# Kernel optimization log

Measured on AMD Instinct MI355X. Metric: run time of the kernel, lower is better.

Reference implementation:

```python
import jax, jax.numpy as jnp
import numpy as np

B, N, HD = 4, 16384, 1024
H, M = 8, 32
D = HD // H  # 128


def setup_inputs() -> dict:
    key = jax.random.key(0)
    ks = jax.random.split(key, 8)
    std = 0.02
    x = jax.random.normal(ks[0], (B, N, HD), dtype=jnp.float32)
    wt_kv_weight = jax.random.normal(ks[1], (2 * HD, HD), dtype=jnp.float32) * std
    wt_kv_bias = jnp.zeros((2 * HD,), dtype=jnp.float32)
    wtq = jax.random.normal(ks[2], (H, M, D), dtype=jnp.float32) * std
    wtq_bias = jnp.zeros((H, M), dtype=jnp.float32)  # registered buffer, zeros
    qkv_proj = jax.random.normal(ks[3], (H, D, 3 * D), dtype=jnp.float32) * std
    out_weight = jax.random.normal(ks[4], (HD, HD), dtype=jnp.float32) * std
    out_bias = jnp.zeros((HD,), dtype=jnp.float32)
    return {
        'x': x,
        'wt_kv_weight': wt_kv_weight,
        'wt_kv_bias': wt_kv_bias,
        'wtq': wtq,
        'wtq_bias': wtq_bias,
        'qkv_proj': qkv_proj,
        'out_weight': out_weight,
        'out_bias': out_bias,
    }


def reference(x, wt_kv_weight, wt_kv_bias, wtq, wtq_bias, qkv_proj, out_weight, out_bias):
    b, n, hd = x.shape
    h, m, d = wtq.shape
    # wt_kv_proj: Linear(hd, 2hd); torch Linear: x @ W.T + b
    kv = x @ wt_kv_weight.T + wt_kv_bias  # [b, n, 2hd]
    xk, xv = jnp.split(kv, 2, axis=-1)
    xk = xk.reshape(b, n, h, d).transpose(0, 2, 1, 3)  # b h n d
    xv = xv.reshape(b, n, h, d).transpose(0, 2, 1, 3)  # b h n d
    # qk_norm=False -> no normalize
    slice_scores = jnp.einsum('hmd,bhnd->bhmn', wtq, xk)
    slice_weights = jax.nn.softmax(slice_scores, axis=-2)  # softmax over slice axis m
    bias = wtq_bias[..., None]  # [h, m, 1]
    slice_token = jnp.einsum('bhmn,bhnd->bhmd', slice_weights, xv)
    slice_norm = jnp.sum(slice_weights, axis=-1, keepdims=True)  # [b,h,m,1]
    slice_token = slice_token / (slice_norm + 1e-5)
    qkv_token = jnp.einsum('bhmd,hde->bhme', slice_token, qkv_proj)  # e = 3d
    q_tok, k_tok, v_tok = jnp.split(qkv_token, 3, axis=-1)
    scale = d ** (-0.5)
    dots = jnp.einsum('bhqd,bhkd->bhqk', q_tok, k_tok) * scale
    attn_weights = jax.nn.softmax(dots, axis=-1)
    out_token = jnp.einsum('bhqk,bhkd->bhqd', attn_weights, v_tok)
    # scatter back via slice weights
    out = jnp.einsum('bhmd,bhmn->bhnd', out_token, slice_weights)
    out = out.transpose(0, 2, 1, 3).reshape(b, n, hd)
    out = out @ out_weight.T + out_bias  # to_out linear (dropout=0)
    temperature = jnp.asarray(1.0, dtype=x.dtype)
    return (out, slice_weights, temperature, bias, attn_weights)
```

## Files before the change

### kernel.cpp

```cpp
#include <hip/hip_runtime.h>
#include <hip/hip_bf16.h>
#include <stdint.h>

#define BB 4
#define NN 16384
#define HDIM 1024
#define HH 8
#define MM 32
#define DD 128

typedef unsigned int u32;
typedef unsigned short u16;
typedef __attribute__((ext_vector_type(8))) short short8;
typedef __attribute__((ext_vector_type(4))) float f32x4;

__device__ __forceinline__ float bf2f(u16 v) {
    union { u32 u; float f; } c; c.u = ((u32)v) << 16; return c.f;
}
__device__ __forceinline__ u16 f2bf(float f) {
    union { float f; u32 u; } c; c.f = f;
    u32 r = c.u + 0x7fffu + ((c.u >> 16) & 1u);
    return (u16)(r >> 16);
}

__device__ __forceinline__ void gload16(const u16* g, u16* l) {
    __builtin_amdgcn_global_load_lds(
        (const __attribute__((address_space(1))) void*)g,
        (__attribute__((address_space(3))) void*)l, 16, 0, 0);
}

#define MFMA16(a, b, c) __builtin_amdgcn_mfma_f32_16x16x32_bf16(a, b, c, 0, 0, 0)

__global__ __launch_bounds__(256) void convert_kernel(const float* __restrict__ x,
                                                      u16* __restrict__ xb, u16* __restrict__ xbT,
                                                      const float* __restrict__ wtq_bias,
                                                      float* __restrict__ out_misc) {
    __shared__ u32 tl[128 * 65];
    const int t = threadIdx.x;
    const int eb = blockIdx.x & 7;
    const int nb = blockIdx.x >> 3;
    const size_t n0 = (size_t)nb * 128;
    const int e0 = eb * 128;

#pragma unroll 4
    for (int i = 0; i < 32; i++) {
        const int idx = t + i * 256;
        const int nl = idx >> 6, e2 = idx & 63;
        const float2 v = *(const float2*)&x[(n0 + nl) * 1024 + e0 + e2 * 2];
        const u32 pk = (u32)f2bf(v.x) | ((u32)f2bf(v.y) << 16);
        ((u32*)xb)[((n0 + nl) * 1024 + e0) / 2 + e2] = pk;
        tl[nl * 65 + e2] = pk;
    }
    __syncthreads();
    const int b = (int)(n0 >> 14);
    const int nloc = (int)(n0 & 16383);
#pragma unroll 4
    for (int i = 0; i < 32; i++) {
        const int idx = t + i * 256;
        const int el = idx >> 6, n2 = idx & 63;
        const u32 w0 = tl[(2 * n2) * 65 + (el >> 1)];
        const u32 w1 = tl[(2 * n2 + 1) * 65 + (el >> 1)];
        const int sh = (el & 1) * 16;
        const u32 o = ((w0 >> sh) & 0xffffu) | (((w1 >> sh) & 0xffffu) << 16);
        ((u32*)xbT)[((size_t)(b * 1024 + e0 + el) * 16384 + nloc + 2 * n2) >> 1] = o;
    }
    if (blockIdx.x == 0) {
        if (t == 0) out_misc[0] = 1.0f;
        if (t < HH * MM) out_misc[1 + t] = wtq_bias[t];
    }
}

__global__ __launch_bounds__(256) void wq_kernel(const float* __restrict__ wtq,
                                                 const float* __restrict__ wkv,
                                                 const float* __restrict__ bkv,
                                                 u16* __restrict__ WQb, float* __restrict__ wqbias,
                                                 u16* __restrict__ wvb) {
    __shared__ float wtql[MM * DD];
    const int ec = blockIdx.x, h = blockIdx.y, t = threadIdx.x;
    for (int i = t; i < MM * DD; i += 256) wtql[i] = wtq[(size_t)h * MM * DD + i];
    __syncthreads();
    const int m = t >> 3;
    const int e = ec * 128 + (t & 7) * 16;
    float acc[16];
#pragma unroll
    for (int j = 0; j < 16; j++) acc[j] = 0.f;
    for (int d = 0; d < DD; d++) {
        const float wv = wtql[m * DD + d];
        const float4* row = (const float4*)(wkv + (size_t)(h * DD + d) * HDIM + e);
#pragma unroll
        for (int j4 = 0; j4 < 4; j4++) {
            float4 v = row[j4];
            acc[j4 * 4 + 0] += wv * v.x; acc[j4 * 4 + 1] += wv * v.y;
            acc[j4 * 4 + 2] += wv * v.z; acc[j4 * 4 + 3] += wv * v.w;
        }
    }
    u32 pk[8];
#pragma unroll
    for (int p = 0; p < 8; p++)
        pk[p] = (u32)f2bf(acc[2 * p]) | ((u32)f2bf(acc[2 * p + 1]) << 16);
    u16* dst = WQb + (size_t)(h * MM + m) * HDIM + e;
#pragma unroll
    for (int p = 0; p < 2; p++) {
        uint4 q4; q4.x = pk[4 * p]; q4.y = pk[4 * p + 1]; q4.z = pk[4 * p + 2]; q4.w = pk[4 * p + 3];
        *(uint4*)&dst[p * 8] = q4;
    }
    if (ec == 0 && t < MM) {
        float s = 0.f;
        for (int d = 0; d < DD; d++) s += wtql[t * DD + d] * bkv[h * DD + d];
        wqbias[h * MM + t] = s;
    }
    {
        const int blk = blockIdx.y * 8 + blockIdx.x;
        const float4* src = (const float4*)(wkv + (size_t)1024 * 1024);
        for (int i = t; i < 4096; i += 256) {
            const int idx4 = blk * 4096 + i;
            float4 v = src[idx4];
            ushort4 o; o.x = f2bf(v.x); o.y = f2bf(v.y); o.z = f2bf(v.z); o.w = f2bf(v.w);
            ((ushort4*)wvb)[idx4] = o;
        }
    }
}

__global__ __launch_bounds__(512, 1) void gemm_score_sm(
        const u16* __restrict__ A, const u16* __restrict__ Bm,
        const float* __restrict__ bias,
        float* __restrict__ sw_out, u16* __restrict__ wN, u16* __restrict__ wT,
        float* __restrict__ pnorm) {
    __shared__ u16 smem[65536];
    const int t = threadIdx.x, l = t & 63, w = t >> 6;
    const int wr = w >> 2, wc = w & 3;

    const int nwg = gridDim.x, cpx = nwg >> 3, bid = blockIdx.x;
    const int tm = (bid & 7) * cpx + (bid >> 3);

    f32x4 acc[8][4];
    const f32x4 zero = {0.f, 0.f, 0.f, 0.f};
#pragma unroll
    for (int mi = 0; mi < 8; mi++)
#pragma unroll
        for (int ni = 0; ni < 4; ni++) acc[mi][ni] = zero;

    const int srow = w * 8 + (l >> 3);
    const int skel = ((l & 7) ^ ((l >> 3) & 7)) * 8;
    const u16* gA = A  + (size_t)(tm * 256 + srow) * 1024 + skel;
    const u16* gB = Bm + (size_t)srow * 1024 + skel;
    const int ldo = w * 512 + l * 8;

#define LAp(SL, H) (&smem[(SL) * 16384 + (H) * 8192])
#define LBp(SL, H) (&smem[32768 + (SL) * 16384 + (H) * 8192])
#define STAGE_A(T, H) { const u16* g_ = gA + (size_t)((H) * 128) * 1024 + (T) * 64; \
    u16* d_ = LAp((T) & 1, H) + ldo; gload16(g_, d_); gload16(g_ + (size_t)64 * 1024, d_ + 4096); }
#define STAGE_B(T, H) { const u16* g_ = gB + (size_t)((H) * 128) * 1024 + (T) * 64; \
    u16* d_ = LBp((T) & 1, H) + ldo; gload16(g_, d_); gload16(g_ + (size_t)64 * 1024, d_ + 4096); }

    const int m16 = l & 15;
    const int ck0 = (((l >> 4) + 0) ^ (l & 7)) << 3;
    const int ck1 = (((l >> 4) + 4) ^ (l & 7)) << 3;
    const int brb = (wc & 1) * 64;
    const int nT = 16;

    STAGE_A(0, 0); STAGE_A(0, 1); STAGE_B(0, 0); STAGE_B(0, 1);
    STAGE_B(1, 0); STAGE_B(1, 1);
    asm volatile("s_waitcnt vmcnt(4)" ::: "memory");
    __builtin_amdgcn_s_barrier();

    for (int kt = 0; kt < nT; ++kt) {
        const int sl = kt & 1;
        const u16* lA = LAp(sl, wr);
        const u16* lB = LBp(sl, wc >> 1);
        short8 aF[4][2], bF[4][2];

#pragma unroll
        for (int fr = 0; fr < 4; fr++) {
            aF[fr][0] = *(const short8*)&lA[(fr * 16 + m16) * 64 + ck0];
            aF[fr][1] = *(const short8*)&lA[(fr * 16 + m16) * 64 + ck1];
        }
#pragma unroll
        for (int fc = 0; fc < 2; fc++) {
            bF[fc][0] = *(const short8*)&lB[(brb + fc * 16 + m16) * 64 + ck0];
            bF[fc][1] = *(const short8*)&lB[(brb + fc * 16 + m16) * 64 + ck1];
        }
        if (kt + 1 < nT) STAGE_A(kt + 1, 0);
        __builtin_amdgcn_s_barrier();
        asm volatile("s_waitcnt lgkmcnt(0)" ::: "memory");
        __builtin_amdgcn_s_setprio(1);
#pragma unroll
        for (int kk = 0; kk < 2; kk++)
#pragma unroll
            for (int mi = 0; mi < 4; mi++) {
                acc[mi][0] = MFMA16(aF[mi][kk], bF[0][kk], acc[mi][0]);
                acc[mi][1] = MFMA16(aF[mi][kk], bF[1][kk], acc[mi][1]);
            }
        __builtin_amdgcn_s_setprio(0);
        __builtin_amdgcn_s_barrier();

#pragma unroll
        for (int fc = 2; fc < 4; fc++) {
            bF[fc][0] = *(const short8*)&lB[(brb + fc * 16 + m16) * 64 + ck0];
            bF[fc][1] = *(const short8*)&lB[(brb + fc * 16 + m16) * 64 + ck1];
        }
        if (kt + 1 < nT) STAGE_A(kt + 1, 1);
        __builtin_amdgcn_s_barrier();
        asm volatile("s_waitcnt lgkmcnt(0)" ::: "memory");
        __builtin_amdgcn_s_setprio(1);
#pragma unroll
        for (int kk = 0; kk < 2; kk++)
#pragma unroll
            for (int mi = 0; mi < 4; mi++) {
                acc[mi][2] = MFMA16(aF[mi][kk], bF[2][kk], acc[mi][2]);
                acc[mi][3] = MFMA16(aF[mi][kk], bF[3][kk], acc[mi][3]);
            }
        __builtin_amdgcn_s_setprio(0);
        __builtin_amdgcn_s_barrier();

#pragma unroll
        for (int fr = 0; fr < 4; fr++) {
            aF[fr][0] = *(const short8*)&lA[((fr + 4) * 16 + m16) * 64 + ck0];
            aF[fr][1] = *(const short8*)&lA[((fr + 4) * 16 + m16) * 64 + ck1];
        }
        if (kt + 2 < nT) STAGE_B(kt + 2, 0);
        __builtin_amdgcn_s_barrier();
        asm volatile("s_waitcnt lgkmcnt(0)" ::: "memory");
        __builtin_amdgcn_s_setprio(1);
#pragma unroll
        for (int kk = 0; kk < 2; kk++)
#pragma unroll
            for (int mi = 0; mi < 4; mi++) {
                acc[4 + mi][0] = MFMA16(aF[mi][kk], bF[0][kk], acc[4 + mi][0]);
                acc[4 + mi][1] = MFMA16(aF[mi][kk], bF[1][kk], acc[4 + mi][1]);
            }
        __builtin_amdgcn_s_setprio(0);
        __builtin_amdgcn_s_barrier();

        if (kt + 2 < nT) STAGE_B(kt + 2, 1);
        __builtin_amdgcn_s_barrier();
        __builtin_amdgcn_s_setprio(1);
#pragma unroll
        for (int kk = 0; kk < 2; kk++)
#pragma unroll
            for (int mi = 0; mi < 4; mi++) {
                acc[4 + mi][2] = MFMA16(aF[mi][kk], bF[2][kk], acc[4 + mi][2]);
                acc[4 + mi][3] = MFMA16(aF[mi][kk], bF[3][kk], acc[4 + mi][3]);
            }
        __builtin_amdgcn_s_setprio(0);
        if (kt < nT - 1) {
            if (kt + 2 < nT) asm volatile("s_waitcnt vmcnt(4)" ::: "memory");
            else             asm volatile("s_waitcnt vmcnt(0)" ::: "memory");
            __builtin_amdgcn_s_barrier();
        }
    }
#undef STAGE_A
#undef STAGE_B
#undef LAp
#undef LBp

    __syncthreads();
    const int cr = (l >> 4) * 4;
    const int cc = l & 15;
#pragma unroll
    for (int ni = 0; ni < 4; ni++) {
        const int hm = wc * 64 + ni * 16 + cc;
        const float bv = bias[hm];
#pragma unroll
        for (int mi = 0; mi < 8; mi++) {
            const int nb_ = wr * 128 + mi * 16 + cr;
            u32 lo = (u32)f2bf(acc[mi][ni][0] + bv) | ((u32)f2bf(acc[mi][ni][1] + bv) << 16);
            u32 hi = (u32)f2bf(acc[mi][ni][2] + bv) | ((u32)f2bf(acc[mi][ni][3] + bv) << 16);
            uint2 pk; pk.x = lo; pk.y = hi;
            *(uint2*)&smem[hm * 256 + (((nb_ >> 2) ^ (hm & 63)) << 2)] = pk;
        }
    }
    __syncthreads();

    const int b = tm >> 6, g = tm & 63;
    const int n_ = t & 255, hs = (t >> 8) * 4;
    const size_t gn = (size_t)g * 256 + n_;
    for (int h = hs; h < hs + 4; h++) {
        float sv[MM];
#pragma unroll
        for (int m = 0; m < MM; m++) {
            const int hm = h * 32 + m;
            sv[m] = bf2f(smem[hm * 256 + (((n_ >> 2) ^ (hm & 63)) << 2) + (n_ & 3)]);
        }
        float mx = sv[0];
#pragma unroll
        for (int m = 1; m < MM; m++) mx = fmaxf(mx, sv[m]);
        float sum = 0.f;
#pragma unroll
        for (int m = 0; m < MM; m++) { sv[m] = __expf(sv[m] - mx); sum += sv[m]; }
        const float inv = 1.f / sum;
        u32 wpk[16];
#pragma unroll
        for (int m = 0; m < MM; m++) {
            const float wv = sv[m] * inv;
            const int hm = h * 32 + m;
            const size_t row = (size_t)(b * 256 + hm);
            sw_out[row * NN + gn] = wv;
            const u16 wb = f2bf(wv);
            wN[row * NN + gn] = wb;
            smem[hm * 256 + (((n_ >> 2) ^ (hm & 63)) << 2) + (n_ & 3)] = wb;
            if (m & 1) wpk[m >> 1] |= ((u32)wb << 16); else wpk[m >> 1] = (u32)wb;
        }
        u16* wrow = wT + ((size_t)(b * NN) + gn) * 256 + h * 32;
#pragma unroll
        for (int p = 0; p < 4; p++) {
            uint4 q4; q4.x = wpk[4 * p]; q4.y = wpk[4 * p + 1]; q4.z = wpk[4 * p + 2]; q4.w = wpk[4 * p + 3];
            *(uint4*)&wrow[p * 8] = q4;
        }
    }
    __syncthreads();

    {
        const int hm2 = t >> 1, half = t & 1;
        float s = 0.f;
        for (int j = 0; j < 128; j++) {
            const int n2 = half * 128 + j;
            s += bf2f(smem[hm2 * 256 + (((n2 >> 2) ^ (hm2 & 63)) << 2) + (n2 & 3)]);
        }
        s += __shfl_xor(s, 1);
        if (half == 0)
            pnorm[((size_t)(b * 8 + (hm2 >> 5)) * 64 + g) * MM + (hm2 & 31)] = s;
    }
}

template<int MODE>
__global__ __launch_bounds__(512, 1) void gemm_nt(
        const u16* __restrict__ A, const u16* __restrict__ Bm,
        const float* __restrict__ bias, void* __restrict__ Cout,
        int NCols, int Kd, int ldk, int ntn, int bofs, int bshift,
        long long bstrideB, long long kCstride) {
    __shared__ u16 ldsA[2][2][8192];
    __shared__ u16 ldsB[2][2][8192];
    const int t = threadIdx.x, l = t & 63, w = t >> 6;
    const int wr = w >> 2, wc = w & 3;

    const int nwg = gridDim.x, cpx = nwg >> 3, bid = blockIdx.x;
    const int swz = (nwg >= 8) ? ((bid & 7) * cpx + (bid >> 3)) : bid;
    const int tm = swz / ntn, tn = swz % ntn;
    const int ks = blockIdx.y;
    const u16* Bb = Bm + (size_t)(tm >> bshift) * bstrideB;

    f32x4 acc[8][4];
    const f32x4 zero = {0.f, 0.f, 0.f, 0.f};
#pragma unroll
    for (int mi = 0; mi < 8; mi++)
#pragma unroll
        for (int ni = 0; ni < 4; ni++) acc[mi][ni] = zero;

    const int srow = w * 8 + (l >> 3);
    const int skel = ((l & 7) ^ ((l >> 3) & 7)) * 8;
    const u16* gA = A  + (size_t)(tm * 256 + srow) * ldk + (size_t)ks * Kd + skel;
    const u16* gB = Bb + (size_t)(tn * 256 + srow) * ldk + (size_t)ks * Kd + skel;
    const int ldo = w * 512 + l * 8;

#define STAGE_A(T, H) { const u16* g_ = gA + (size_t)((H) * 128) * ldk + (T) * 64; \
    u16* d_ = &ldsA[(T) & 1][H][ldo]; gload16(g_, d_); gload16(g_ + (size_t)64 * ldk, d_ + 4096); }
#define STAGE_B(T, H) { const u16* g_ = gB + (size_t)((H) * 128) * ldk + (T) * 64; \
    u16* d_ = &ldsB[(T) & 1][H][ldo]; gload16(g_, d_); gload16(g_ + (size_t)64 * ldk, d_ + 4096); }

    const int m16 = l & 15;
    const int ck0 = (((l >> 4) + 0) ^ (l & 7)) << 3;
    const int ck1 = (((l >> 4) + 4) ^ (l & 7)) << 3;
    const int brb = (wc & 1) * 64;
    const int nT = Kd >> 6;

    STAGE_A(0, 0); STAGE_A(0, 1); STAGE_B(0, 0); STAGE_B(0, 1);
    STAGE_B(1, 0); STAGE_B(1, 1);
    asm volatile("s_waitcnt vmcnt(4)" ::: "memory");
    __builtin_amdgcn_s_barrier();

    for (int kt = 0; kt < nT; ++kt) {
        const int sl = kt & 1;
        const u16* lA = ldsA[sl][wr];
        const u16* lB = ldsB[sl][wc >> 1];
        short8 aF[4][2], bF[4][2];

#pragma unroll
        for (int fr = 0; fr < 4; fr++) {
            aF[fr][0] = *(const short8*)&lA[(fr * 16 + m16) * 64 + ck0];
            aF[fr][1] = *(const short8*)&lA[(fr * 16 + m16) * 64 + ck1];
        }
#pragma unroll
        for (int fc = 0; fc < 2; fc++) {
            bF[fc][0] = *(const short8*)&lB[(brb + fc * 16 + m16) * 64 + ck0];
            bF[fc][1] = *(const short8*)&lB[(brb + fc * 16 + m16) * 64 + ck1];
        }
        if (kt + 1 < nT) STAGE_A(kt + 1, 0);
        __builtin_amdgcn_s_barrier();
        asm volatile("s_waitcnt lgkmcnt(0)" ::: "memory");
        __builtin_amdgcn_s_setprio(1);
#pragma unroll
        for (int kk = 0; kk < 2; kk++)
#pragma unroll
            for (int mi = 0; mi < 4; mi++) {
                acc[mi][0] = MFMA16(aF[mi][kk], bF[0][kk], acc[mi][0]);
                acc[mi][1] = MFMA16(aF[mi][kk], bF[1][kk], acc[mi][1]);
            }
        __builtin_amdgcn_s_setprio(0);
        __builtin_amdgcn_s_barrier();

#pragma unroll
        for (int fc = 2; fc < 4; fc++) {
            bF[fc][0] = *(const short8*)&lB[(brb + fc * 16 + m16) * 64 + ck0];
            bF[fc][1] = *(const short8*)&lB[(brb + fc * 16 + m16) * 64 + ck1];
        }
        if (kt + 1 < nT) STAGE_A(kt + 1, 1);
        __builtin_amdgcn_s_barrier();
        asm volatile("s_waitcnt lgkmcnt(0)" ::: "memory");
        __builtin_amdgcn_s_setprio(1);
#pragma unroll
        for (int kk = 0; kk < 2; kk++)
#pragma unroll
            for (int mi = 0; mi < 4; mi++) {
                acc[mi][2] = MFMA16(aF[mi][kk], bF[2][kk], acc[mi][2]);
                acc[mi][3] = MFMA16(aF[mi][kk], bF[3][kk], acc[mi][3]);
            }
        __builtin_amdgcn_s_setprio(0);
        __builtin_amdgcn_s_barrier();

#pragma unroll
        for (int fr = 0; fr < 4; fr++) {
            aF[fr][0] = *(const short8*)&lA[((fr + 4) * 16 + m16) * 64 + ck0];
            aF[fr][1] = *(const short8*)&lA[((fr + 4) * 16 + m16) * 64 + ck1];
        }
        if (kt + 2 < nT) STAGE_B(kt + 2, 0);
        __builtin_amdgcn_s_barrier();
        asm volatile("s_waitcnt lgkmcnt(0)" ::: "memory");
        __builtin_amdgcn_s_setprio(1);
#pragma unroll
        for (int kk = 0; kk < 2; kk++)
#pragma unroll
            for (int mi = 0; mi < 4; mi++) {
                acc[4 + mi][0] = MFMA16(aF[mi][kk], bF[0][kk], acc[4 + mi][0]);
                acc[4 + mi][1] = MFMA16(aF[mi][kk], bF[1][kk], acc[4 + mi][1]);
            }
        __builtin_amdgcn_s_setprio(0);
        __builtin_amdgcn_s_barrier();

        if (kt + 2 < nT) STAGE_B(kt + 2, 1);
        __builtin_amdgcn_s_barrier();
        __builtin_amdgcn_s_setprio(1);
#pragma unroll
        for (int kk = 0; kk < 2; kk++)
#pragma unroll
            for (int mi = 0; mi < 4; mi++) {
                acc[4 + mi][2] = MFMA16(aF[mi][kk], bF[2][kk], acc[4 + mi][2]);
                acc[4 + mi][3] = MFMA16(aF[mi][kk], bF[3][kk], acc[4 + mi][3]);
            }
        __builtin_amdgcn_s_setprio(0);
        if (kt < nT - 1) {
            if (kt + 2 < nT) asm volatile("s_waitcnt vmcnt(4)" ::: "memory");
            else             asm volatile("s_waitcnt vmcnt(0)" ::: "memory");
            __builtin_amdgcn_s_barrier();
        }
    }
#undef STAGE_A
#undef STAGE_B

    const int cr = (l >> 4) * 4;
    const int cc = l & 15;
    if (MODE == 2) {
        u16* Cp = (u16*)Cout + (size_t)ks * kCstride;
#pragma unroll
        for (int ni = 0; ni < 4; ni++) {
            const int col = tn * 256 + wc * 64 + ni * 16 + cc;
            const float bv = bias ? bias[col] : 0.0f;
#pragma unroll
            for (int mi = 0; mi < 8; mi++) {
                const int row0 = tm * 256 + wr * 128 + mi * 16 + cr;
#pragma unroll
                for (int q = 0; q < 4; q++)
                    Cp[(size_t)(row0 + q) * NCols + col] = f2bf(acc[mi][ni][q] + bv);
            }
        }
    } else {
        float* Cp = (float*)Cout + (size_t)ks * kCstride;
#pragma unroll
        for (int ni = 0; ni < 4; ni++) {
            const int col = tn * 256 + wc * 64 + ni * 16 + cc;
            const float bv = bias ? bias[col] : 0.0f;
#pragma unroll
            for (int mi = 0; mi < 8; mi++) {
                const int row0 = tm * 256 + wr * 128 + mi * 16 + cr;
#pragma unroll
                for (int q = 0; q < 4; q++)
                    Cp[(size_t)(row0 + q) * NCols + col] = acc[mi][ni][q] + bv;
            }
        }
    }
}

__global__ __launch_bounds__(256, 2) void gemm_small(
        const u16* __restrict__ A, const u16* __restrict__ Bm,
        const float* __restrict__ bias, float* __restrict__ Cout,
        int Ncols, int Kds, int ldk, int ntn, int bshift,
        long long bstrideB, long long kCstride) {
    __shared__ u16 lds_a[128 * 32];
    __shared__ u16 lds_b[128 * 32];
    const int t = threadIdx.x, l = t & 63, w = t >> 6;
    const int wr = w >> 1, wc = w & 1;

    const int nwg = gridDim.x, cpx = nwg >> 3, bid = blockIdx.x;
    const int swz = (nwg >= 8) ? ((bid & 7) * cpx + (bid >> 3)) : bid;
    const int tm = swz / ntn, tn = swz % ntn;
    const int ks = blockIdx.y;
    const u16* Bb = Bm + (size_t)(tm >> bshift) * bstrideB;

    f32x4 acc[4][4];
    const f32x4 zero = {0.f, 0.f, 0.f, 0.f};
#pragma unroll
    for (int mi = 0; mi < 4; mi++)
#pragma unroll
        for (int ni = 0; ni < 4; ni++) acc[mi][ni] = zero;

    const int srow = w * 32 + (l >> 2);
    const int scol = (l & 3) * 8;
    const u16* ga = A  + (size_t)(tm * 128 + srow) * ldk + (size_t)ks * Kds + scol;
    const u16* gb = Bb + (size_t)(tn * 128 + srow) * ldk + (size_t)ks * Kds + scol;
    u16* la = &lds_a[(w * 32) * 32];
    u16* lb = &lds_b[(w * 32) * 32];
    const size_t rstep = (size_t)16 * ldk;

    const int nK = Kds >> 5;
    const int kg = (l >> 4) * 8;
    const int ra = wr * 64 + (l & 15);
    const int rb = wc * 64 + (l & 15);

    for (int kt = 0; kt < nK; kt++) {
        __syncthreads();
        const int ko = kt << 5;
        gload16(ga + ko,         la);
        gload16(ga + ko + rstep, la + 16 * 32);
        gload16(gb + ko,         lb);
        gload16(gb + ko + rstep, lb + 16 * 32);
        __syncthreads();

        short8 af[4], bfr[4];
#pragma unroll
        for (int mi = 0; mi < 4; mi++) af[mi] = *(const short8*)&lds_a[(ra + mi * 16) * 32 + kg];
#pragma unroll
        for (int ni = 0; ni < 4; ni++) bfr[ni] = *(const short8*)&lds_b[(rb + ni * 16) * 32 + kg];
#pragma unroll
        for (int mi = 0; mi < 4; mi++)
#pragma unroll
            for (int ni = 0; ni < 4; ni++)
                acc[mi][ni] = MFMA16(af[mi], bfr[ni], acc[mi][ni]);
    }

    float* Cp = Cout + (size_t)ks * kCstride;
#pragma unroll
    for (int ni = 0; ni < 4; ni++) {
        const int col = tn * 128 + wc * 64 + ni * 16 + (l & 15);
        const float bv = bias ? bias[col] : 0.0f;
#pragma unroll
        for (int mi = 0; mi < 4; mi++) {
            const int row0 = tm * 128 + wr * 64 + mi * 16 + ((l >> 4) << 2);
#pragma unroll
            for (int q = 0; q < 4; q++)
                Cp[(size_t)(row0 + q) * Ncols + col] = acc[mi][ni][q] + bv;
        }
    }
}

__global__ __launch_bounds__(256) void sum_U(const u16* __restrict__ U_part, u16* __restrict__ U2) {
    const int i = blockIdx.x * 256 + threadIdx.x;
    float4 s = make_float4(0.f, 0.f, 0.f, 0.f);
    for (int ks = 0; ks < 16; ks++) {
        const ushort4 v = ((const ushort4*)(U_part + (size_t)ks * 1048576))[i];
        s.x += bf2f(v.x); s.y += bf2f(v.y); s.z += bf2f(v.z); s.w += bf2f(v.w);
    }
    const int r = i >> 8, e4 = i & 255;
    const int b = r >> 8, h = (r >> 5) & 7, m = r & 31;
    const int r2 = h * 128 + b * 32 + m;
    ushort4 o; o.x = f2bf(s.x); o.y = f2bf(s.y); o.z = f2bf(s.z); o.w = f2bf(s.w);
    ((ushort4*)U2)[r2 * 256 + e4] = o;
}

__global__ __launch_bounds__(256) void st_fix(const float* __restrict__ C2,
                                              const float* __restrict__ pnorm,
                                              const float* __restrict__ bkv,
                                              u16* __restrict__ st_red) {
    __shared__ float norm[MM];
    const int bh = blockIdx.x, b = bh >> 3, h = bh & 7, t = threadIdx.x;
    if (t < MM) {
        float s = 0.f;
        for (int g = 0; g < 64; g++) s += pnorm[((size_t)bh * 64 + g) * MM + t];
        norm[t] = s;
    }
    __syncthreads();
#pragma unroll
    for (int i = 0; i < 16; i++) {
        const int idx = t * 16 + i;
        const int m = idx >> 7, d = idx & 127;
        const float nv = norm[m];
        float c = 0.f;
        const size_t off = (size_t)(h * 128 + d) * 128 + b * 32 + m;
#pragma unroll
        for (int ks = 0; ks < 8; ks++) c += C2[(size_t)ks * 131072 + off];
        const float v = (c + bkv[1024 + h * 128 + d] * nv) / (nv + 1e-5f);
        st_red[(size_t)bh * 4096 + idx] = f2bf(v);
    }
}

__global__ __launch_bounds__(256) void qt_kernel(const u16* __restrict__ st_red,
                                                 const float* __restrict__ qkvp,
                                                 float* __restrict__ qt_g) {
    __shared__ u16 st_lds[MM * DD];
    const int es = blockIdx.x, bh = blockIdx.y, h = bh & 7, t = threadIdx.x;
    {
        const uint4* src = (const uint4*)(st_red + (size_t)bh * 4096);
        ((uint4*)st_lds)[t] = src[t];
        ((uint4*)st_lds)[t + 256] = src[t + 256];
    }
    __syncthreads();
    const float* qw = qkvp + (size_t)h * DD * 384;
#pragma unroll
    for (int i = 0; i < 4; i++) {
        const int idx = t + i * 256;
        const int m = idx >> 5, el = idx & 31;
        const int e = es * 32 + el;
        float s = 0.f;
        for (int d = 0; d < DD; d++) s += bf2f(st_lds[m * DD + d]) * qw[d * 384 + e];
        qt_g[((size_t)bh * MM + m) * 384 + e] = s;
    }
}

__global__ void finalize2_kernel(const float* __restrict__ qt_g,
                                 float* __restrict__ attn_out, float* __restrict__ otw) {
    __shared__ float qt[MM * 384];
    __shared__ float dots[MM * MM];
    const int bh = blockIdx.x, t = threadIdx.x;

#pragma unroll
    for (int i = 0; i < 48; i++) qt[t + i * 256] = qt_g[(size_t)bh * 12288 + t + i * 256];
    __syncthreads();
    const float scale = 0.08838834764831845f;
#pragma unroll
    for (int i = 0; i < 4; i++) {
        int idx = t * 4 + i;
        int qi = idx >> 5, kj = idx & 31;
        float s = 0.f;
        for (int d = 0; d < DD; d++) s += qt[qi * 384 + d] * qt[kj * 384 + 128 + d];
        dots[idx] = s * scale;
    }
    __syncthreads();
    if (t < MM) {
        float mx = -1e30f;
        float ex[MM];
#pragma unroll
        for (int j = 0; j < MM; j++) mx = fmaxf(mx, dots[t * MM + j]);
        float sm = 0.f;
#pragma unroll
        for (int j = 0; j < MM; j++) { ex[j] = __expf(dots[t * MM + j] - mx); sm += ex[j]; }
        float inv = 1.f / sm;
#pragma unroll
        for (int j = 0; j < MM; j++) {
            float v = ex[j] * inv;
            dots[t * MM + j] = v;
            attn_out[((size_t)bh * MM + t) * MM + j] = v;
        }
    }
    __syncthreads();
#pragma unroll
    for (int i = 0; i < 16; i++) {
        int e = t + i * 256;
        int m = e >> 7, d = e & 127;
        float s = 0.f;
#pragma unroll
        for (int j = 0; j < MM; j++) s += dots[m * MM + j] * qt[j * 384 + 256 + d];
        otw[(size_t)bh * 4096 + e] = s;
    }
}

__global__ __launch_bounds__(256) void zmat_kernel(const float* __restrict__ otw,
                                                   const float* __restrict__ outw,
                                                   u16* __restrict__ Zt) {
    __shared__ float ot_lds[MM * DD];
    const int bh = blockIdx.y, b = bh >> 3, h = bh & 7;
    const int es = blockIdx.x;
    const int t = threadIdx.x;
    for (int i = t; i < MM * DD; i += 256) ot_lds[i] = otw[(size_t)bh * 4096 + i];
    __syncthreads();
    const int e = es * 128 + (t >> 1);
    const int m0 = (t & 1) * 16;
    const float* ow = outw + (size_t)e * HDIM + h * DD;
    float acc[16];
#pragma unroll
    for (int m = 0; m < 16; m++) acc[m] = 0.f;
    for (int d = 0; d < DD; d += 4) {
        float4 o4 = *(const float4*)&ow[d];
#pragma unroll
        for (int m = 0; m < 16; m++) {
            const float* otr = &ot_lds[(m0 + m) * DD + d];
            acc[m] += o4.x * otr[0] + o4.y * otr[1] + o4.z * otr[2] + o4.w * otr[3];
        }
    }
    u32 pk[8];
#pragma unroll
    for (int p = 0; p < 8; p++)
        pk[p] = (u32)f2bf(acc[2 * p]) | ((u32)f2bf(acc[2 * p + 1]) << 16);
    u16* dst = Zt + ((size_t)b * 1024 + e) * 256 + h * MM + m0;
#pragma unroll
    for (int p = 0; p < 2; p++) {
        uint4 q4; q4.x = pk[4 * p]; q4.y = pk[4 * p + 1]; q4.z = pk[4 * p + 2]; q4.w = pk[4 * p + 3];
        *(uint4*)&dst[p * 8] = q4;
    }
}

extern "C" void kernel_launch(void* const* d_in, const int* in_sizes, int n_in,
                              void* d_out, int out_size, void* d_ws, size_t ws_size,
                              hipStream_t stream) {
    const float* x        = (const float*)d_in[0];
    const float* wkv      = (const float*)d_in[1];
    const float* bkv      = (const float*)d_in[2];
    const float* wtq      = (const float*)d_in[3];
    const float* wtq_bias = (const float*)d_in[4];
    const float* qkvp     = (const float*)d_in[5];
    const float* outw     = (const float*)d_in[6];
    const float* outb     = (const float*)d_in[7];

    float* out  = (float*)d_out;
    float* out0 = out;
    float* out1 = out + 67108864;
    float* out2 = out + 83886080;
    float* out4 = out + 83886337;

    char* ws = (char*)d_ws;
    u16*   xb     = (u16*)(ws);
    u16*   xbT    = (u16*)(ws + 134217728);
    u16*   wN     = (u16*)(ws + 268435456);
    u16*   wT     = (u16*)(ws + 301989888);
    u16*   U_part = (u16*)(ws + 335544320);
    u16*   U2     = (u16*)(ws + 402653184);
    float* C2     = (float*)(ws + 404750336);
    u16*   wvb    = (u16*)(ws + 409468928);
    u16*   WQb    = (u16*)(ws + 411566080);
    float* wqbias = (float*)(ws + 412090368);
    float* pnorm  = (float*)(ws + 412091392);
    u16*   st_red = (u16*)(ws + 412353536);
    float* otws   = (float*)(ws + 412615680);
    u16*   Zt     = (u16*)(ws + 413138944);
    float* qt_g   = (float*)(ws + 415236096);

    convert_kernel<<<dim3(4096), dim3(256), 0, stream>>>(x, xb, xbT, wtq_bias, out2);
    wq_kernel<<<dim3(8, 8), dim3(256), 0, stream>>>(wtq, wkv, bkv, WQb, wqbias, wvb);
    gemm_score_sm<<<dim3(256), dim3(512), 0, stream>>>(xb, WQb, wqbias, out1, wN, wT, pnorm);
    gemm_nt<2><<<dim3(16, 16), dim3(512), 0, stream>>>(wN, xbT, nullptr, (void*)U_part,
                                                       1024, 1024, 16384, 4, 0, 0,
                                                       (long long)16777216, (long long)1048576);
    sum_U<<<dim3(1024), dim3(256), 0, stream>>>(U_part, U2);
    gemm_small<<<dim3(8, 8), dim3(256), 0, stream>>>(wvb, U2, nullptr, C2,
                                                     128, 128, 1024, 1, 0,
                                                     (long long)131072, (long long)131072);
    st_fix<<<dim3(32), dim3(256), 0, stream>>>(C2, pnorm, bkv, st_red);
    qt_kernel<<<dim3(12, 32), dim3(256), 0, stream>>>(st_red, qkvp, qt_g);
    finalize2_kernel<<<dim3(32), dim3(256), 0, stream>>>(qt_g, out4, otws);
    zmat_kernel<<<dim3(8, 32), dim3(256), 0, stream>>>(otws, outw, Zt);
    gemm_small<<<dim3(4096), dim3(256), 0, stream>>>(wT, Zt, outb, out0,
                                                     1024, 256, 256, 8, 7,
                                                     (long long)262144, 0);
}
```

Baseline: 505.2 us.

## Fuse partial-sum reduction, value projection and normalization into one slice-token kernel

```diff
diff --git a/kernel.cpp b/kernel.cpp
--- a/kernel.cpp
+++ b/kernel.cpp
@@ -562,44 +562,73 @@
     }
 }
 
-__global__ __launch_bounds__(256) void sum_U(const u16* __restrict__ U_part, u16* __restrict__ U2) {
-    const int i = blockIdx.x * 256 + threadIdx.x;
-    float4 s = make_float4(0.f, 0.f, 0.f, 0.f);
-    for (int ks = 0; ks < 16; ks++) {
-        const ushort4 v = ((const ushort4*)(U_part + (size_t)ks * 1048576))[i];
-        s.x += bf2f(v.x); s.y += bf2f(v.y); s.z += bf2f(v.z); s.w += bf2f(v.w);
-    }
-    const int r = i >> 8, e4 = i & 255;
-    const int b = r >> 8, h = (r >> 5) & 7, m = r & 31;
-    const int r2 = h * 128 + b * 32 + m;
-    ushort4 o; o.x = f2bf(s.x); o.y = f2bf(s.y); o.z = f2bf(s.z); o.w = f2bf(s.w);
-    ((ushort4*)U2)[r2 * 256 + e4] = o;
-}
-
-__global__ __launch_bounds__(256) void st_fix(const float* __restrict__ C2,
-                                              const float* __restrict__ pnorm,
-                                              const float* __restrict__ bkv,
-                                              u16* __restrict__ st_red) {
+__global__ __launch_bounds__(256) void stmat_kernel(
+        const u16* __restrict__ U_part, const u16* __restrict__ wvb,
+        const float* __restrict__ pnorm, const float* __restrict__ bkv,
+        u16* __restrict__ st_red) {
+    __shared__ u16 u_lds[32 * 1024];
+    __shared__ u16 wv_lds[128 * 32];
     __shared__ float norm[MM];
-    const int bh = blockIdx.x, b = bh >> 3, h = bh & 7, t = threadIdx.x;
+    const int bh = blockIdx.x, b = bh >> 3, h = bh & 7;
+    const int t = threadIdx.x, l = t & 63, w = t >> 6;
+
     if (t < MM) {
         float s = 0.f;
         for (int g = 0; g < 64; g++) s += pnorm[((size_t)bh * 64 + g) * MM + t];
         norm[t] = s;
     }
-    __syncthreads();
-#pragma unroll
-    for (int i = 0; i < 16; i++) {
-        const int idx = t * 16 + i;
-        const int m = idx >> 7, d = idx & 127;
-        const float nv = norm[m];
-        float c = 0.f;
-        const size_t off = (size_t)(h * 128 + d) * 128 + b * 32 + m;
-#pragma unroll
-        for (int ks = 0; ks < 8; ks++) c += C2[(size_t)ks * 131072 + off];
-        const float v = (c + bkv[1024 + h * 128 + d] * nv) / (nv + 1e-5f);
-        st_red[(size_t)bh * 4096 + idx] = f2bf(v);
-    }
+    for (int m = 0; m < MM; m++) {
+        const u16* src = U_part + ((size_t)(b * 256 + h * 32 + m)) * 1024 + t * 4;
+        float4 s = make_float4(0.f, 0.f, 0.f, 0.f);
+#pragma unroll
+        for (int ks = 0; ks < 16; ks++) {
+            const ushort4 v = *(const ushort4*)(src + (size_t)ks * 1048576);
+            s.x += bf2f(v.x); s.y += bf2f(v.y); s.z += bf2f(v.z); s.w += bf2f(v.w);
+        }
+        ushort4 o; o.x = f2bf(s.x); o.y = f2bf(s.y); o.z = f2bf(s.z); o.w = f2bf(s.w);
+        const int phys = (t >> 1) ^ (m & 7);
+        *(ushort4*)&u_lds[m * 1024 + phys * 8 + (t & 1) * 4] = o;
+    }
+
+    f32x4 acc[2][2];
+    const f32x4 zero = {0.f, 0.f, 0.f, 0.f};
+    acc[0][0] = zero; acc[0][1] = zero; acc[1][0] = zero; acc[1][1] = zero;
+    const int m16 = l & 15, kg = (l >> 4) * 8;
+
+    for (int kt = 0; kt < 32; kt++) {
+        __syncthreads();
+        {
+            const u16* src = wvb + (size_t)(h * 128 + (t >> 2)) * 1024 + kt * 32 + (t & 3) * 8;
+            gload16(src, wv_lds + w * 512 + l * 8);
+            gload16(src + (size_t)64 * 1024, wv_lds + 2048 + w * 512 + l * 8);
+        }
+        __syncthreads();
+
+        short8 a0 = *(const short8*)&wv_lds[(w * 32 + m16) * 32 + kg];
+        short8 a1 = *(const short8*)&wv_lds[(w * 32 + 16 + m16) * 32 + kg];
+        const int c0 = (((kt * 4 + (l >> 4)) ^ (m16 & 7)) << 3);
+        short8 b0 = *(const short8*)&u_lds[m16 * 1024 + c0];
+        short8 b1 = *(const short8*)&u_lds[(16 + m16) * 1024 + c0];
+        acc[0][0] = MFMA16(a0, b0, acc[0][0]);
+        acc[0][1] = MFMA16(a0, b1, acc[0][1]);
+        acc[1][0] = MFMA16(a1, b0, acc[1][0]);
+        acc[1][1] = MFMA16(a1, b1, acc[1][1]);
+    }
+
+    const int cr = (l >> 4) << 2;
+    const int cc = l & 15;
+#pragma unroll
+    for (int df = 0; df < 2; df++)
+#pragma unroll
+        for (int mf = 0; mf < 2; mf++)
+#pragma unroll
+            for (int q = 0; q < 4; q++) {
+                const int d = w * 32 + df * 16 + cr + q;
+                const int m = mf * 16 + cc;
+                const float nv = norm[m];
+                const float v = (acc[df][mf][q] + bkv[1024 + h * 128 + d] * nv) / (nv + 1e-5f);
+                st_red[(size_t)bh * 4096 + m * 128 + d] = f2bf(v);
+            }
 }
 
 __global__ __launch_bounds__(256) void qt_kernel(const u16* __restrict__ st_red,
@@ -632,7 +661,8 @@
     const int bh = blockIdx.x, t = threadIdx.x;
 
 #pragma unroll
-    for (int i = 0; i < 48; i++) qt[t + i * 256] = qt_g[(size_t)bh * 12288 + t + i * 256];
+    for (int i = 0; i < 12; i++)
+        ((float4*)qt)[t + i * 256] = ((const float4*)(qt_g + (size_t)bh * 12288))[t + i * 256];
     __syncthreads();
     const float scale = 0.08838834764831845f;
 #pragma unroll
@@ -731,8 +761,6 @@
     u16*   wN     = (u16*)(ws + 268435456);
     u16*   wT     = (u16*)(ws + 301989888);
     u16*   U_part = (u16*)(ws + 335544320);
-    u16*   U2     = (u16*)(ws + 402653184);
-    float* C2     = (float*)(ws + 404750336);
     u16*   wvb    = (u16*)(ws + 409468928);
     u16*   WQb    = (u16*)(ws + 411566080);
     float* wqbias = (float*)(ws + 412090368);
@@ -748,11 +776,7 @@
     gemm_nt<2><<<dim3(16, 16), dim3(512), 0, stream>>>(wN, xbT, nullptr, (void*)U_part,
                                                        1024, 1024, 16384, 4, 0, 0,
                                                        (long long)16777216, (long long)1048576);
-    sum_U<<<dim3(1024), dim3(256), 0, stream>>>(U_part, U2);
-    gemm_small<<<dim3(8, 8), dim3(256), 0, stream>>>(wvb, U2, nullptr, C2,
-                                                     128, 128, 1024, 1, 0,
-                                                     (long long)131072, (long long)131072);
-    st_fix<<<dim3(32), dim3(256), 0, stream>>>(C2, pnorm, bkv, st_red);
+    stmat_kernel<<<dim3(32), dim3(256), 0, stream>>>(U_part, wvb, pnorm, bkv, st_red);
     qt_kernel<<<dim3(12, 32), dim3(256), 0, stream>>>(st_red, qkvp, qt_g);
     finalize2_kernel<<<dim3(32), dim3(256), 0, stream>>>(qt_g, out4, otws);
     zmat_kernel<<<dim3(8, 32), dim3(256), 0, stream>>>(otws, outw, Zt);
```

Result: no change. 510.9 us (+1.1%).
